# Kernel tuning notes

Measured on AMD Instinct MI355X. Metric: run time of the kernel, lower is better.

Reference implementation:

```python
import jax, jax.numpy as jnp
import numpy as np

B, L, D, H = 8, 1024, 1024, 16
DPH = D // H  # 64


def setup_inputs() -> dict:
    key = jax.random.key(0)
    ks = jax.random.split(key, 12)
    s = 1.0 / np.sqrt(D)
    return {
        "key": jax.random.normal(ks[0], (B, L, D), jnp.float32),
        "value": jax.random.normal(ks[1], (B, L, D), jnp.float32),
        "query": jax.random.normal(ks[2], (B, L, D), jnp.float32),
        "attn_mask": jax.random.randint(ks[3], (B, L, L), 0, 2) > 0,
        "Wq": jax.random.normal(ks[4], (D, D), jnp.float32) * s,
        "bq": jnp.zeros((D,), jnp.float32),
        "Wk": jax.random.normal(ks[5], (D, D), jnp.float32) * s,
        "bk": jnp.zeros((D,), jnp.float32),
        "Wv": jax.random.normal(ks[6], (D, D), jnp.float32) * s,
        "bv": jnp.zeros((D,), jnp.float32),
        "Wo": jax.random.normal(ks[7], (D, D), jnp.float32) * s,
        "bo": jnp.zeros((D,), jnp.float32),
        "gamma": jnp.ones((D,), jnp.float32),
        "beta": jnp.zeros((D,), jnp.float32),
    }


def _layer_norm(x, gamma, beta, eps=1e-5):
    mu = jnp.mean(x, axis=-1, keepdims=True)
    var = jnp.var(x, axis=-1, keepdims=True)
    return (x - mu) * jax.lax.rsqrt(var + eps) * gamma + beta


def reference(key, value, query, attn_mask, Wq, bq, Wk, bk, Wv, bv, Wo, bo, gamma, beta):
    residual = query
    k = key @ Wk + bk      # [B, L, D]
    v = value @ Wv + bv
    q = query @ Wq + bq
    # faithful to torch: raw row-major view into [B*H, L, dph] (NOT standard head transpose)
    k = k.reshape(B * H, -1, DPH)
    v = v.reshape(B * H, -1, DPH)
    q = q.reshape(B * H, -1, DPH)
    # faithful to torch repeat: tile whole batch H times along dim 0
    mask = jnp.tile(attn_mask, (H, 1, 1))  # [B*H, L, L]
    scale = DPH ** (-0.5)
    scores = jnp.einsum('bqd,bkd->bqk', q, k) * scale
    scores = jnp.where(mask, jnp.float32(-1e9), scores)
    attention = jax.nn.softmax(scores, axis=2)
    context = jnp.einsum('bqk,bkd->bqd', attention, v)  # [B*H, L, dph]
    context = context.reshape(B, -1, D)
    output = context @ Wo + bo
    output = _layer_norm(residual + output, gamma, beta)
    return (output, attention)
```

## Files before the change

### kernel.cpp

```cpp
#include <hip/hip_runtime.h>

typedef __attribute__((ext_vector_type(8))) short short8;
typedef __attribute__((ext_vector_type(4))) float f32x4;

#define AS1C(p) ((const __attribute__((address_space(1))) void*)(p))
#define AS3(p)  ((__attribute__((address_space(3))) void*)(p))

__device__ __forceinline__ unsigned short f2bf(float f) {
  unsigned int u = __float_as_uint(f);
  return (unsigned short)((u + 0x7fffu + ((u >> 16) & 1u)) >> 16);
}

__device__ __forceinline__ void gload16(const void* g, void* l) {
  __builtin_amdgcn_global_load_lds(AS1C(g), AS3(l), 16, 0, 0);
}

#define EXP_C 0.18033688011112042f

__global__ __launch_bounds__(256) void conv_bf16(const float* __restrict__ in,
                                                 unsigned short* __restrict__ out, int n4) {
  int i = blockIdx.x * 256 + threadIdx.x;
  if (i >= n4) return;
  float4 v = ((const float4*)in)[i];
  ushort4 o;
  o.x = f2bf(v.x); o.y = f2bf(v.y); o.z = f2bf(v.z); o.w = f2bf(v.w);
  ((ushort4*)out)[i] = o;
}

__global__ __launch_bounds__(256) void pack_mask_kernel(const int* __restrict__ m,
                                                        unsigned int* __restrict__ bits) {
  int i = blockIdx.x * 256 + threadIdx.x;
  unsigned long long b = __ballot(m[i] != 0);
  if ((threadIdx.x & 63) == 0) {
    bits[(i >> 5)]     = (unsigned int)b;
    bits[(i >> 5) + 1] = (unsigned int)(b >> 32);
  }
}

__global__ __launch_bounds__(256) void transpose_w(const float* __restrict__ W0,
                                                   const float* __restrict__ W1,
                                                   const float* __restrict__ W2,
                                                   const float* __restrict__ W3,
                                                   unsigned short* __restrict__ WtBase) {
  __shared__ float t[32][33];
  const float* W = (blockIdx.z == 0) ? W0 : (blockIdx.z == 1) ? W1 : (blockIdx.z == 2) ? W2 : W3;
  unsigned short* Wt = WtBase + (size_t)blockIdx.z * 1024 * 1024;
  int bx = blockIdx.x * 32, by = blockIdx.y * 32;
  int tx = threadIdx.x & 31, ty = threadIdx.x >> 5;
#pragma unroll
  for (int i = 0; i < 4; ++i) {
    int r = ty + i * 8;
    t[r][tx] = W[(size_t)(by + r) * 1024 + bx + tx];
  }
  __syncthreads();
#pragma unroll
  for (int i = 0; i < 4; ++i) {
    int r = ty + i * 8;
    Wt[(size_t)(bx + r) * 1024 + by + tx] = f2bf(t[tx][r]);
  }
}

__global__ __launch_bounds__(256) void transpose_v(const unsigned short* __restrict__ v,
                                                   unsigned short* __restrict__ vt) {
  __shared__ unsigned short t[32][33];
  int b = blockIdx.z;
  int bx = blockIdx.x * 32;
  int by = blockIdx.y * 32;
  int tx = threadIdx.x & 31, ty = threadIdx.x >> 5;
#pragma unroll
  for (int i = 0; i < 4; ++i) {
    int r = ty + i * 8;
    t[r][tx] = v[(size_t)b * 65536 + (size_t)(by + r) * 64 + bx + tx];
  }
  __syncthreads();
#pragma unroll
  for (int i = 0; i < 4; ++i) {
    int r = ty + i * 8;
    vt[(size_t)b * 65536 + (size_t)(bx + r) * 1024 + by + tx] = t[tx][r];
  }
}

template <int MODE>
__global__ __launch_bounds__(256) void gemm_bf16_kernel(
    const unsigned short* __restrict__ A, const unsigned short* __restrict__ Bt,
    const float* __restrict__ bias, const float* __restrict__ res,
    unsigned short* __restrict__ Cb, float* __restrict__ Cf) {
  const int K = 1024, N = 1024;
  __shared__ unsigned short lA[128 * 32];
  __shared__ unsigned short lB[128 * 32];
  const int tid = threadIdx.x;
  const int wave = tid >> 6, lane = tid & 63;
  const int row_l = lane & 15, kg = lane >> 4;
  const int wg = blockIdx.y * 8 + blockIdx.x;
  const int idx = (wg & 7) * 64 + (wg >> 3);
  const int m0 = (idx >> 3) * 128, n0 = (idx & 7) * 128;
  const int wm = (wave >> 1) * 64, wn = (wave & 1) * 64;
  f32x4 acc[4][4] = {};

  for (int k0 = 0; k0 < K; k0 += 32) {
    __syncthreads();
#pragma unroll
    for (int it = 0; it < 2; ++it) {
      int c = wave * 64 + it * 256 + lane;
      int r = c >> 2, ch = c & 3;
      int sch = ch ^ (r & 3);
      gload16(A + (size_t)(m0 + r) * K + k0 + sch * 8, lA + (wave * 64 + it * 256) * 8);
      gload16(Bt + (size_t)(n0 + r) * K + k0 + sch * 8, lB + (wave * 64 + it * 256) * 8);
    }
    __syncthreads();
    short8 af[4], bfr[4];
#pragma unroll
    for (int t = 0; t < 4; ++t) {
      int ra = wm + t * 16 + row_l;
      af[t] = *(const short8*)(lA + ra * 32 + ((kg ^ (ra & 3)) << 3));
      int rb = wn + t * 16 + row_l;
      bfr[t] = *(const short8*)(lB + rb * 32 + ((kg ^ (rb & 3)) << 3));
    }
    __builtin_amdgcn_s_setprio(1);
#pragma unroll
    for (int mt = 0; mt < 4; ++mt)
#pragma unroll
      for (int nt = 0; nt < 4; ++nt)
        acc[mt][nt] = __builtin_amdgcn_mfma_f32_16x16x32_bf16(af[mt], bfr[nt], acc[mt][nt], 0, 0, 0);
    __builtin_amdgcn_s_setprio(0);
  }
#pragma unroll
  for (int mt = 0; mt < 4; ++mt)
#pragma unroll
    for (int nt = 0; nt < 4; ++nt)
#pragma unroll
      for (int r = 0; r < 4; ++r) {
        int grow = m0 + wm + mt * 16 + kg * 4 + r;
        int gcol = n0 + wn + nt * 16 + row_l;
        float v = acc[mt][nt][r] + bias[gcol];
        if (MODE == 0) {
          Cb[(size_t)grow * N + gcol] = f2bf(v);
        } else {
          v += res[(size_t)grow * N + gcol];
          Cf[(size_t)grow * N + gcol] = v;
        }
      }
}

__global__ __launch_bounds__(256) void attn_kernel(
    const unsigned short* __restrict__ Q,
    const unsigned short* __restrict__ Km,
    const unsigned short* __restrict__ Vt,
    const unsigned int* __restrict__ mbits,
    float* __restrict__ attn,
    unsigned short* __restrict__ ctx) {
  __shared__ unsigned short lQ[64 * 64];
  __shared__ unsigned short lK[64 * 64];
  __shared__ unsigned short lV[64 * 64];
  __shared__ unsigned short lP[64 * 64];
  const int tid = threadIdx.x, wave = tid >> 6, lane = tid & 63;
  const int row_l = lane & 15, kg = lane >> 4;
  const int wg = blockIdx.y * 16 + blockIdx.x;
  const int idx = (wg & 7) * 256 + (wg >> 3);
  const int batch = idx >> 4, qt = idx & 15;
  const int q0 = qt * 64;
  const unsigned short* Qb = Q + (size_t)batch * 65536;
  const unsigned short* Kb = Km + (size_t)batch * 65536;
  const unsigned short* Vb = Vt + (size_t)batch * 65536;
  const unsigned int* mrow = mbits + (size_t)(batch & 7) * 32768;
  float* attb = attn + (size_t)batch * 1048576;

#pragma unroll
  for (int it = 0; it < 2; ++it) {
    int c = wave * 64 + it * 256 + lane;
    int r = c >> 3, ch = c & 7;
    int sch = ch ^ (r & 7);
    gload16(Qb + (size_t)(q0 + r) * 64 + sch * 8, lQ + (wave * 64 + it * 256) * 8);
  }
  __syncthreads();
  short8 qf[2];
  {
    int rq = wave * 16 + row_l;
#pragma unroll
    for (int kk = 0; kk < 2; ++kk)
      qf[kk] = *(const short8*)(lQ + rq * 64 + (((kk * 4 + kg) ^ (rq & 7)) << 3));
  }

  float l_part[4] = {0.f, 0.f, 0.f, 0.f};
  const int qrow_base = q0 + wave * 16 + kg * 4;

  for (int kt = 0; kt < 16; ++kt) {
    __syncthreads();
#pragma unroll
    for (int it = 0; it < 2; ++it) {
      int c = wave * 64 + it * 256 + lane;
      int r = c >> 3, ch = c & 7;
      int sch = ch ^ (r & 7);
      gload16(Kb + (size_t)(kt * 64 + r) * 64 + sch * 8, lK + (wave * 64 + it * 256) * 8);
    }
    __syncthreads();
    f32x4 s[4];
    __builtin_amdgcn_s_setprio(1);
#pragma unroll
    for (int cf = 0; cf < 4; ++cf) {
      int rk = cf * 16 + row_l;
      f32x4 a = {0.f, 0.f, 0.f, 0.f};
#pragma unroll
      for (int kk = 0; kk < 2; ++kk) {
        short8 kf = *(const short8*)(lK + rk * 64 + (((kk * 4 + kg) ^ (rk & 7)) << 3));
        a = __builtin_amdgcn_mfma_f32_16x16x32_bf16(qf[kk], kf, a, 0, 0, 0);
      }
      s[cf] = a;
    }
    __builtin_amdgcn_s_setprio(0);
#pragma unroll
    for (int r = 0; r < 4; ++r) {
      unsigned int w0 = mrow[(qrow_base + r) * 32 + kt * 2];
      unsigned int w1 = mrow[(qrow_base + r) * 32 + kt * 2 + 1];
#pragma unroll
      for (int cf = 0; cf < 4; ++cf) {
        int kl = cf * 16 + row_l;
        unsigned int w = (kl & 32) ? w1 : w0;
        int bit = (w >> (kl & 31)) & 1;
        float e = __builtin_exp2f(s[cf][r] * EXP_C);
        l_part[r] += bit ? 0.f : e;
      }
    }
  }
  float il[4];
#pragma unroll
  for (int r = 0; r < 4; ++r) {
    float se = l_part[r];
#pragma unroll
    for (int sh = 1; sh < 16; sh <<= 1) se += __shfl_xor(se, sh);
    il[r] = 1.f / se;
  }

  f32x4 cacc[4] = {};

  for (int kt = 0; kt < 16; ++kt) {
    __syncthreads();
#pragma unroll
    for (int it = 0; it < 2; ++it) {
      int c = wave * 64 + it * 256 + lane;
      int r = c >> 3, ch = c & 7;
      int sch = ch ^ (r & 7);
      gload16(Kb + (size_t)(kt * 64 + r) * 64 + sch * 8, lK + (wave * 64 + it * 256) * 8);
      gload16(Vb + (size_t)r * 1024 + kt * 64 + sch * 8, lV + (wave * 64 + it * 256) * 8);
    }
    __syncthreads();
    f32x4 s[4];
    __builtin_amdgcn_s_setprio(1);
#pragma unroll
    for (int cf = 0; cf < 4; ++cf) {
      int rk = cf * 16 + row_l;
      f32x4 a = {0.f, 0.f, 0.f, 0.f};
#pragma unroll
      for (int kk = 0; kk < 2; ++kk) {
        short8 kf = *(const short8*)(lK + rk * 64 + (((kk * 4 + kg) ^ (rk & 7)) << 3));
        a = __builtin_amdgcn_mfma_f32_16x16x32_bf16(qf[kk], kf, a, 0, 0, 0);
      }
      s[cf] = a;
    }
    __builtin_amdgcn_s_setprio(0);
#pragma unroll
    for (int r = 0; r < 4; ++r) {
      unsigned int w0 = mrow[(qrow_base + r) * 32 + kt * 2];
      unsigned int w1 = mrow[(qrow_base + r) * 32 + kt * 2 + 1];
      float* arow = attb + (size_t)(qrow_base + r) * 1024 + kt * 64;
      int prow = wave * 16 + kg * 4 + r;
#pragma unroll
      for (int cf = 0; cf < 4; ++cf) {
        int kl = cf * 16 + row_l;
        unsigned int w = (kl & 32) ? w1 : w0;
        int bit = (w >> (kl & 31)) & 1;
        float e = __builtin_exp2f(s[cf][r] * EXP_C) * il[r];
        float p = bit ? 0.f : e;
        __builtin_nontemporal_store(p, arow + kl);
        int pch = (kl >> 3) ^ (prow & 7);
        lP[prow * 64 + pch * 8 + (kl & 7)] = f2bf(p);
      }
    }
    __syncthreads();
    __builtin_amdgcn_s_setprio(1);
#pragma unroll
    for (int kk = 0; kk < 2; ++kk) {
      int rp = wave * 16 + row_l;
      short8 pa = *(const short8*)(lP + rp * 64 + (((kk * 4 + kg) ^ (rp & 7)) << 3));
#pragma unroll
      for (int df = 0; df < 4; ++df) {
        int rv = df * 16 + row_l;
        short8 vb = *(const short8*)(lV + rv * 64 + (((kk * 4 + kg) ^ (rv & 7)) << 3));
        cacc[df] = __builtin_amdgcn_mfma_f32_16x16x32_bf16(pa, vb, cacc[df], 0, 0, 0);
      }
    }
    __builtin_amdgcn_s_setprio(0);
  }
#pragma unroll
  for (int df = 0; df < 4; ++df)
#pragma unroll
    for (int r = 0; r < 4; ++r) {
      int grow = q0 + wave * 16 + kg * 4 + r;
      int gcol = df * 16 + row_l;
      ctx[(size_t)batch * 65536 + (size_t)grow * 64 + gcol] = f2bf(cacc[df][r]);
    }
}

__global__ __launch_bounds__(256) void layernorm_kernel(float* __restrict__ io,
                                                        const float* __restrict__ gamma,
                                                        const float* __restrict__ beta) {
  int wave = threadIdx.x >> 6, lane = threadIdx.x & 63;
  size_t row = (size_t)blockIdx.x * 4 + wave;
  float* p = io + row * 1024;
  float4 v[4];
  float s = 0.f, ss = 0.f;
#pragma unroll
  for (int i = 0; i < 4; ++i) {
    v[i] = ((const float4*)p)[lane + i * 64];
    s += v[i].x + v[i].y + v[i].z + v[i].w;
    ss += v[i].x * v[i].x + v[i].y * v[i].y + v[i].z * v[i].z + v[i].w * v[i].w;
  }
#pragma unroll
  for (int m = 1; m < 64; m <<= 1) { s += __shfl_xor(s, m); ss += __shfl_xor(ss, m); }
  float mu = s * (1.f / 1024.f);
  float var = ss * (1.f / 1024.f) - mu * mu;
  float rinv = rsqrtf(var + 1e-5f);
#pragma unroll
  for (int i = 0; i < 4; ++i) {
    int idx = lane + i * 64;
    float4 g = ((const float4*)gamma)[idx];
    float4 b = ((const float4*)beta)[idx];
    float4 o;
    o.x = (v[i].x - mu) * rinv * g.x + b.x;
    o.y = (v[i].y - mu) * rinv * g.y + b.y;
    o.z = (v[i].z - mu) * rinv * g.z + b.z;
    o.w = (v[i].w - mu) * rinv * g.w + b.w;
    ((float4*)p)[idx] = o;
  }
}

extern "C" void kernel_launch(void* const* d_in, const int* in_sizes, int n_in,
                              void* d_out, int out_size, void* d_ws, size_t ws_size,
                              hipStream_t stream) {
  const float* key   = (const float*)d_in[0];
  const float* value = (const float*)d_in[1];
  const float* query = (const float*)d_in[2];
  const int* amask   = (const int*)d_in[3];
  const float* Wq = (const float*)d_in[4];
  const float* bq = (const float*)d_in[5];
  const float* Wk = (const float*)d_in[6];
  const float* bk = (const float*)d_in[7];
  const float* Wv = (const float*)d_in[8];
  const float* bv = (const float*)d_in[9];
  const float* Wo = (const float*)d_in[10];
  const float* bo = (const float*)d_in[11];
  const float* gamma = (const float*)d_in[12];
  const float* beta  = (const float*)d_in[13];

  char* ws = (char*)d_ws;
  const size_t MB = 1024 * 1024;
  unsigned short* B0 = (unsigned short*)(ws + 0);
  unsigned short* B1 = (unsigned short*)(ws + 16 * MB);
  unsigned short* B2 = (unsigned short*)(ws + 32 * MB);
  unsigned short* B3 = (unsigned short*)(ws + 48 * MB);
  unsigned short* Wts = (unsigned short*)(ws + 64 * MB);
  unsigned int* mbits = (unsigned int*)(ws + 72 * MB);
  unsigned short* Wqt = Wts;
  unsigned short* Wkt = Wts + 1 * MB;
  unsigned short* Wvt = Wts + 2 * MB;
  unsigned short* Wot = Wts + 3 * MB;

  float* out_f = (float*)d_out;
  float* attn_f = (float*)d_out + (size_t)8388608;

  const int n4 = 8388608 / 4;
  dim3 gemm_grid(8, 64);

  transpose_w<<<dim3(32, 32, 4), 256, 0, stream>>>(Wq, Wk, Wv, Wo, Wts);
  pack_mask_kernel<<<32768, 256, 0, stream>>>(amask, mbits);

  conv_bf16<<<8192, 256, 0, stream>>>(query, B0, n4);
  gemm_bf16_kernel<0><<<gemm_grid, 256, 0, stream>>>(B0, Wqt, bq, nullptr, B1, nullptr);
  conv_bf16<<<8192, 256, 0, stream>>>(key, B0, n4);
  gemm_bf16_kernel<0><<<gemm_grid, 256, 0, stream>>>(B0, Wkt, bk, nullptr, B2, nullptr);
  conv_bf16<<<8192, 256, 0, stream>>>(value, B0, n4);
  gemm_bf16_kernel<0><<<gemm_grid, 256, 0, stream>>>(B0, Wvt, bv, nullptr, B3, nullptr);
  transpose_v<<<dim3(2, 32, 128), 256, 0, stream>>>(B3, B0);

  attn_kernel<<<dim3(16, 128), 256, 0, stream>>>(B1, B2, B0, mbits, attn_f, B3);

  gemm_bf16_kernel<1><<<gemm_grid, 256, 0, stream>>>(B3, Wot, bo, query, nullptr, out_f);
  layernorm_kernel<<<2048, 256, 0, stream>>>(out_f, gamma, beta);
}
```

Measured before the change: 360.7 us.

## Double-buffer attention K/V tiles, transpose mask bits, batch QKV GEMMs

Several changes are bundled. The attention kernel double-buffers K and V tiles in LDS so the next tile's loads overlap compute, and it replaces the paired __syncthreads with a vmcnt wait plus barrier. The packed mask is stored transposed so each thread fetches its four rows' words with one vector load. Attention probability writes are staged through LDS as bf16 and written as 16-byte nontemporal stores, which rounds the fp32 attention output to bf16 precision. When the workspace is large enough, the three input conversions and QKV GEMMs are merged into single launches over a z dimension.

Result: slower. 732.3 us (+103.0%).

```diff
diff --git a/kernel.cpp b/kernel.cpp
--- a/kernel.cpp
+++ b/kernel.cpp
@@ -10,6 +10,9 @@
   unsigned int u = __float_as_uint(f);
   return (unsigned short)((u + 0x7fffu + ((u >> 16) & 1u)) >> 16);
 }
+__device__ __forceinline__ float bf2f(short s) {
+  return __uint_as_float(((unsigned int)(unsigned short)s) << 16);
+}
 
 __device__ __forceinline__ void gload16(const void* g, void* l) {
   __builtin_amdgcn_global_load_lds(AS1C(g), AS3(l), 16, 0, 0);
@@ -17,8 +20,14 @@
 
 #define EXP_C 0.18033688011112042f
 
-__global__ __launch_bounds__(256) void conv_bf16(const float* __restrict__ in,
-                                                 unsigned short* __restrict__ out, int n4) {
+__global__ __launch_bounds__(256) void conv3_bf16(const float* __restrict__ s0,
+                                                  const float* __restrict__ s1,
+                                                  const float* __restrict__ s2,
+                                                  unsigned short* __restrict__ d0,
+                                                  unsigned short* __restrict__ d1,
+                                                  unsigned short* __restrict__ d2, int n4) {
+  const float* in = (blockIdx.z == 0) ? s0 : (blockIdx.z == 1) ? s1 : s2;
+  unsigned short* out = (blockIdx.z == 0) ? d0 : (blockIdx.z == 1) ? d1 : d2;
   int i = blockIdx.x * 256 + threadIdx.x;
   if (i >= n4) return;
   float4 v = ((const float4*)in)[i];
@@ -28,12 +37,14 @@
 }
 
 __global__ __launch_bounds__(256) void pack_mask_kernel(const int* __restrict__ m,
-                                                        unsigned int* __restrict__ bits) {
+                                                        unsigned int* __restrict__ bitsT) {
   int i = blockIdx.x * 256 + threadIdx.x;
-  unsigned long long b = __ballot(m[i] != 0);
+  unsigned long long bl = __ballot(m[i] != 0);
   if ((threadIdx.x & 63) == 0) {
-    bits[(i >> 5)]     = (unsigned int)b;
-    bits[(i >> 5) + 1] = (unsigned int)(b >> 32);
+    int b_ = i >> 20, q = (i >> 10) & 1023, k = i & 1023;
+    int w = k >> 5;
+    bitsT[b_ * 32768 + w * 1024 + q]       = (unsigned int)bl;
+    bitsT[b_ * 32768 + (w + 1) * 1024 + q] = (unsigned int)(bl >> 32);
   }
 }
 
@@ -81,13 +92,12 @@
 }
 
 template <int MODE>
-__global__ __launch_bounds__(256) void gemm_bf16_kernel(
+__device__ __forceinline__ void gemm_body(
     const unsigned short* __restrict__ A, const unsigned short* __restrict__ Bt,
     const float* __restrict__ bias, const float* __restrict__ res,
-    unsigned short* __restrict__ Cb, float* __restrict__ Cf) {
+    unsigned short* __restrict__ Cb, float* __restrict__ Cf,
+    unsigned short* lA, unsigned short* lB) {
   const int K = 1024, N = 1024;
-  __shared__ unsigned short lA[128 * 32];
-  __shared__ unsigned short lB[128 * 32];
   const int tid = threadIdx.x;
   const int wave = tid >> 6, lane = tid & 63;
   const int row_l = lane & 15, kg = lane >> 4;
@@ -142,17 +152,39 @@
       }
 }
 
+__global__ __launch_bounds__(256) void gemm_qkv_kernel(
+    const unsigned short* __restrict__ A0, const unsigned short* __restrict__ A1,
+    const unsigned short* __restrict__ A2, const unsigned short* __restrict__ WtBase,
+    const float* __restrict__ b0, const float* __restrict__ b1, const float* __restrict__ b2,
+    unsigned short* __restrict__ C0, unsigned short* __restrict__ C1,
+    unsigned short* __restrict__ C2) {
+  __shared__ unsigned short lA[128 * 32];
+  __shared__ unsigned short lB[128 * 32];
+  int z = blockIdx.z;
+  const unsigned short* A = (z == 0) ? A0 : (z == 1) ? A1 : A2;
+  const float* bias = (z == 0) ? b0 : (z == 1) ? b1 : b2;
+  unsigned short* C = (z == 0) ? C0 : (z == 1) ? C1 : C2;
+  gemm_body<0>(A, WtBase + (size_t)z * 1024 * 1024, bias, nullptr, C, nullptr, lA, lB);
+}
+
+__global__ __launch_bounds__(256) void gemm_out_kernel(
+    const unsigned short* __restrict__ A, const unsigned short* __restrict__ Bt,
+    const float* __restrict__ bias, const float* __restrict__ res, float* __restrict__ Cf) {
+  __shared__ unsigned short lA[128 * 32];
+  __shared__ unsigned short lB[128 * 32];
+  gemm_body<1>(A, Bt, bias, res, nullptr, Cf, lA, lB);
+}
+
 __global__ __launch_bounds__(256) void attn_kernel(
     const unsigned short* __restrict__ Q,
     const unsigned short* __restrict__ Km,
     const unsigned short* __restrict__ Vt,
-    const unsigned int* __restrict__ mbits,
+    const unsigned int* __restrict__ mbitsT,
     float* __restrict__ attn,
     unsigned short* __restrict__ ctx) {
-  __shared__ unsigned short lQ[64 * 64];
-  __shared__ unsigned short lK[64 * 64];
-  __shared__ unsigned short lV[64 * 64];
-  __shared__ unsigned short lP[64 * 64];
+  __shared__ unsigned short lQP[64 * 64];
+  __shared__ unsigned short lK[2][64 * 64];
+  __shared__ unsigned short lV[2][64 * 64];
   const int tid = threadIdx.x, wave = tid >> 6, lane = tid & 63;
   const int row_l = lane & 15, kg = lane >> 4;
   const int wg = blockIdx.y * 16 + blockIdx.x;
@@ -162,38 +194,57 @@
   const unsigned short* Qb = Q + (size_t)batch * 65536;
   const unsigned short* Kb = Km + (size_t)batch * 65536;
   const unsigned short* Vb = Vt + (size_t)batch * 65536;
-  const unsigned int* mrow = mbits + (size_t)(batch & 7) * 32768;
+  const unsigned int* mT = mbitsT + (size_t)(batch & 7) * 32768;
   float* attb = attn + (size_t)batch * 1048576;
+  const int qrow_base = q0 + wave * 16 + kg * 4;
+
+#define STAGE_K(kt, buf)                                                              \
+  {                                                                                   \
+    _Pragma("unroll") for (int it = 0; it < 2; ++it) {                                \
+      int c = wave * 64 + it * 256 + lane;                                            \
+      int r_ = c >> 3, ch_ = c & 7, sch_ = ch_ ^ (r_ & 7);                            \
+      gload16(Kb + (size_t)((kt) * 64 + r_) * 64 + sch_ * 8,                          \
+              lK[buf] + (wave * 64 + it * 256) * 8);                                  \
+    }                                                                                 \
+  }
+#define STAGE_V(kt, buf)                                                              \
+  {                                                                                   \
+    _Pragma("unroll") for (int it = 0; it < 2; ++it) {                                \
+      int c = wave * 64 + it * 256 + lane;                                            \
+      int r_ = c >> 3, ch_ = c & 7, sch_ = ch_ ^ (r_ & 7);                            \
+      gload16(Vb + (size_t)r_ * 1024 + (kt) * 64 + sch_ * 8,                          \
+              lV[buf] + (wave * 64 + it * 256) * 8);                                  \
+    }                                                                                 \
+  }
+#define WAIT_BAR                                              \
+  asm volatile("s_waitcnt vmcnt(0)" ::: "memory");            \
+  __builtin_amdgcn_s_barrier();
 
 #pragma unroll
   for (int it = 0; it < 2; ++it) {
     int c = wave * 64 + it * 256 + lane;
     int r = c >> 3, ch = c & 7;
     int sch = ch ^ (r & 7);
-    gload16(Qb + (size_t)(q0 + r) * 64 + sch * 8, lQ + (wave * 64 + it * 256) * 8);
-  }
-  __syncthreads();
+    gload16(Qb + (size_t)(q0 + r) * 64 + sch * 8, lQP + (wave * 64 + it * 256) * 8);
+  }
+  STAGE_K(0, 0)
+  WAIT_BAR
   short8 qf[2];
   {
     int rq = wave * 16 + row_l;
 #pragma unroll
     for (int kk = 0; kk < 2; ++kk)
-      qf[kk] = *(const short8*)(lQ + rq * 64 + (((kk * 4 + kg) ^ (rq & 7)) << 3));
+      qf[kk] = *(const short8*)(lQP + rq * 64 + (((kk * 4 + kg) ^ (rq & 7)) << 3));
   }
 
   float l_part[4] = {0.f, 0.f, 0.f, 0.f};
-  const int qrow_base = q0 + wave * 16 + kg * 4;
 
   for (int kt = 0; kt < 16; ++kt) {
-    __syncthreads();
-#pragma unroll
-    for (int it = 0; it < 2; ++it) {
-      int c = wave * 64 + it * 256 + lane;
-      int r = c >> 3, ch = c & 7;
-      int sch = ch ^ (r & 7);
-      gload16(Kb + (size_t)(kt * 64 + r) * 64 + sch * 8, lK + (wave * 64 + it * 256) * 8);
-    }
-    __syncthreads();
+    int cur = kt & 1;
+    if (kt < 15) STAGE_K(kt + 1, cur ^ 1)
+    uint4 mw0 = *(const uint4*)(mT + (kt * 2 + 0) * 1024 + qrow_base);
+    uint4 mw1 = *(const uint4*)(mT + (kt * 2 + 1) * 1024 + qrow_base);
+    unsigned int wv[2][4] = {{mw0.x, mw0.y, mw0.z, mw0.w}, {mw1.x, mw1.y, mw1.z, mw1.w}};
     f32x4 s[4];
     __builtin_amdgcn_s_setprio(1);
 #pragma unroll
@@ -202,25 +253,21 @@
       f32x4 a = {0.f, 0.f, 0.f, 0.f};
 #pragma unroll
       for (int kk = 0; kk < 2; ++kk) {
-        short8 kf = *(const short8*)(lK + rk * 64 + (((kk * 4 + kg) ^ (rk & 7)) << 3));
+        short8 kf = *(const short8*)(lK[cur] + rk * 64 + (((kk * 4 + kg) ^ (rk & 7)) << 3));
         a = __builtin_amdgcn_mfma_f32_16x16x32_bf16(qf[kk], kf, a, 0, 0, 0);
       }
       s[cf] = a;
     }
     __builtin_amdgcn_s_setprio(0);
 #pragma unroll
-    for (int r = 0; r < 4; ++r) {
-      unsigned int w0 = mrow[(qrow_base + r) * 32 + kt * 2];
-      unsigned int w1 = mrow[(qrow_base + r) * 32 + kt * 2 + 1];
+    for (int r = 0; r < 4; ++r)
 #pragma unroll
       for (int cf = 0; cf < 4; ++cf) {
-        int kl = cf * 16 + row_l;
-        unsigned int w = (kl & 32) ? w1 : w0;
-        int bit = (w >> (kl & 31)) & 1;
+        int bit = (wv[cf >> 1][r] >> ((cf & 1) * 16 + row_l)) & 1;
         float e = __builtin_exp2f(s[cf][r] * EXP_C);
         l_part[r] += bit ? 0.f : e;
       }
-    }
+    WAIT_BAR
   }
   float il[4];
 #pragma unroll
@@ -232,18 +279,20 @@
   }
 
   f32x4 cacc[4] = {};
-
+  unsigned short* lP = lQP;
+
+  STAGE_K(0, 0)
+  STAGE_V(0, 0)
+  WAIT_BAR
   for (int kt = 0; kt < 16; ++kt) {
-    __syncthreads();
-#pragma unroll
-    for (int it = 0; it < 2; ++it) {
-      int c = wave * 64 + it * 256 + lane;
-      int r = c >> 3, ch = c & 7;
-      int sch = ch ^ (r & 7);
-      gload16(Kb + (size_t)(kt * 64 + r) * 64 + sch * 8, lK + (wave * 64 + it * 256) * 8);
-      gload16(Vb + (size_t)r * 1024 + kt * 64 + sch * 8, lV + (wave * 64 + it * 256) * 8);
-    }
-    __syncthreads();
+    int cur = kt & 1;
+    if (kt < 15) {
+      STAGE_K(kt + 1, cur ^ 1)
+      STAGE_V(kt + 1, cur ^ 1)
+    }
+    uint4 mw0 = *(const uint4*)(mT + (kt * 2 + 0) * 1024 + qrow_base);
+    uint4 mw1 = *(const uint4*)(mT + (kt * 2 + 1) * 1024 + qrow_base);
+    unsigned int wv[2][4] = {{mw0.x, mw0.y, mw0.z, mw0.w}, {mw1.x, mw1.y, mw1.z, mw1.w}};
     f32x4 s[4];
     __builtin_amdgcn_s_setprio(1);
 #pragma unroll
@@ -252,7 +301,7 @@
       f32x4 a = {0.f, 0.f, 0.f, 0.f};
 #pragma unroll
       for (int kk = 0; kk < 2; ++kk) {
-        short8 kf = *(const short8*)(lK + rk * 64 + (((kk * 4 + kg) ^ (rk & 7)) << 3));
+        short8 kf = *(const short8*)(lK[cur] + rk * 64 + (((kk * 4 + kg) ^ (rk & 7)) << 3));
         a = __builtin_amdgcn_mfma_f32_16x16x32_bf16(qf[kk], kf, a, 0, 0, 0);
       }
       s[cf] = a;
@@ -260,23 +309,33 @@
     __builtin_amdgcn_s_setprio(0);
 #pragma unroll
     for (int r = 0; r < 4; ++r) {
-      unsigned int w0 = mrow[(qrow_base + r) * 32 + kt * 2];
-      unsigned int w1 = mrow[(qrow_base + r) * 32 + kt * 2 + 1];
-      float* arow = attb + (size_t)(qrow_base + r) * 1024 + kt * 64;
       int prow = wave * 16 + kg * 4 + r;
 #pragma unroll
       for (int cf = 0; cf < 4; ++cf) {
         int kl = cf * 16 + row_l;
-        unsigned int w = (kl & 32) ? w1 : w0;
-        int bit = (w >> (kl & 31)) & 1;
+        int bit = (wv[cf >> 1][r] >> ((cf & 1) * 16 + row_l)) & 1;
         float e = __builtin_exp2f(s[cf][r] * EXP_C) * il[r];
         float p = bit ? 0.f : e;
-        __builtin_nontemporal_store(p, arow + kl);
         int pch = (kl >> 3) ^ (prow & 7);
         lP[prow * 64 + pch * 8 + (kl & 7)] = f2bf(p);
       }
     }
-    __syncthreads();
+    {
+      int pr = wave * 16 + kg * 4 + (row_l & 3);
+      int cb = row_l >> 2;
+      float* arow = attb + (size_t)(q0 + pr) * 1024 + kt * 64 + cb * 16;
+      int ch0 = (cb * 2) ^ (pr & 7), ch1 = (cb * 2 + 1) ^ (pr & 7);
+      short8 a0 = *(const short8*)(lP + pr * 64 + ch0 * 8);
+      short8 a1 = *(const short8*)(lP + pr * 64 + ch1 * 8);
+      f32x4 o0 = {bf2f(a0[0]), bf2f(a0[1]), bf2f(a0[2]), bf2f(a0[3])};
+      f32x4 o1 = {bf2f(a0[4]), bf2f(a0[5]), bf2f(a0[6]), bf2f(a0[7])};
+      f32x4 o2 = {bf2f(a1[0]), bf2f(a1[1]), bf2f(a1[2]), bf2f(a1[3])};
+      f32x4 o3 = {bf2f(a1[4]), bf2f(a1[5]), bf2f(a1[6]), bf2f(a1[7])};
+      __builtin_nontemporal_store(o0, (f32x4*)arow + 0);
+      __builtin_nontemporal_store(o1, (f32x4*)arow + 1);
+      __builtin_nontemporal_store(o2, (f32x4*)arow + 2);
+      __builtin_nontemporal_store(o3, (f32x4*)arow + 3);
+    }
     __builtin_amdgcn_s_setprio(1);
 #pragma unroll
     for (int kk = 0; kk < 2; ++kk) {
@@ -285,11 +344,12 @@
 #pragma unroll
       for (int df = 0; df < 4; ++df) {
         int rv = df * 16 + row_l;
-        short8 vb = *(const short8*)(lV + rv * 64 + (((kk * 4 + kg) ^ (rv & 7)) << 3));
+        short8 vb = *(const short8*)(lV[cur] + rv * 64 + (((kk * 4 + kg) ^ (rv & 7)) << 3));
         cacc[df] = __builtin_amdgcn_mfma_f32_16x16x32_bf16(pa, vb, cacc[df], 0, 0, 0);
       }
     }
     __builtin_amdgcn_s_setprio(0);
+    WAIT_BAR
   }
 #pragma unroll
   for (int df = 0; df < 4; ++df)
@@ -299,6 +359,9 @@
       int gcol = df * 16 + row_l;
       ctx[(size_t)batch * 65536 + (size_t)grow * 64 + gcol] = f2bf(cacc[df][r]);
     }
+#undef STAGE_K
+#undef STAGE_V
+#undef WAIT_BAR
 }
 
 __global__ __launch_bounds__(256) void layernorm_kernel(float* __restrict__ io,
@@ -354,36 +417,50 @@
 
   char* ws = (char*)d_ws;
   const size_t MB = 1024 * 1024;
-  unsigned short* B0 = (unsigned short*)(ws + 0);
-  unsigned short* B1 = (unsigned short*)(ws + 16 * MB);
-  unsigned short* B2 = (unsigned short*)(ws + 32 * MB);
-  unsigned short* B3 = (unsigned short*)(ws + 48 * MB);
-  unsigned short* Wts = (unsigned short*)(ws + 64 * MB);
-  unsigned int* mbits = (unsigned int*)(ws + 72 * MB);
-  unsigned short* Wqt = Wts;
-  unsigned short* Wkt = Wts + 1 * MB;
-  unsigned short* Wvt = Wts + 2 * MB;
-  unsigned short* Wot = Wts + 3 * MB;
-
   float* out_f = (float*)d_out;
   float* attn_f = (float*)d_out + (size_t)8388608;
-
   const int n4 = 8388608 / 4;
   dim3 gemm_grid(8, 64);
-
-  transpose_w<<<dim3(32, 32, 4), 256, 0, stream>>>(Wq, Wk, Wv, Wo, Wts);
-  pack_mask_kernel<<<32768, 256, 0, stream>>>(amask, mbits);
-
-  conv_bf16<<<8192, 256, 0, stream>>>(query, B0, n4);
-  gemm_bf16_kernel<0><<<gemm_grid, 256, 0, stream>>>(B0, Wqt, bq, nullptr, B1, nullptr);
-  conv_bf16<<<8192, 256, 0, stream>>>(key, B0, n4);
-  gemm_bf16_kernel<0><<<gemm_grid, 256, 0, stream>>>(B0, Wkt, bk, nullptr, B2, nullptr);
-  conv_bf16<<<8192, 256, 0, stream>>>(value, B0, n4);
-  gemm_bf16_kernel<0><<<gemm_grid, 256, 0, stream>>>(B0, Wvt, bv, nullptr, B3, nullptr);
-  transpose_v<<<dim3(2, 32, 128), 256, 0, stream>>>(B3, B0);
-
-  attn_kernel<<<dim3(16, 128), 256, 0, stream>>>(B1, B2, B0, mbits, attn_f, B3);
-
-  gemm_bf16_kernel<1><<<gemm_grid, 256, 0, stream>>>(B3, Wot, bo, query, nullptr, out_f);
-  layernorm_kernel<<<2048, 256, 0, stream>>>(out_f, gamma, beta);
-}
+  dim3 gemm_grid3(8, 64, 3);
+
+  const bool fused = ws_size >= 106 * MB;
+  if (fused) {
+    unsigned short* A0 = (unsigned short*)(ws + 0);
+    unsigned short* A1 = (unsigned short*)(ws + 16 * MB);
+    unsigned short* A2 = (unsigned short*)(ws + 32 * MB);
+    unsigned short* B1 = (unsigned short*)(ws + 48 * MB);
+    unsigned short* B2 = (unsigned short*)(ws + 64 * MB);
+    unsigned short* B3 = (unsigned short*)(ws + 80 * MB);
+    unsigned short* Wts = (unsigned short*)(ws + 96 * MB);
+    unsigned int* mbitsT = (unsigned int*)(ws + 104 * MB);
+
+    transpose_w<<<dim3(32, 32, 4), 256, 0, stream>>>(Wq, Wk, Wv, Wo, Wts);
+    pack_mask_kernel<<<32768, 256, 0, stream>>>(amask, mbitsT);
+    conv3_bf16<<<dim3(8192, 1, 3), 256, 0, stream>>>(query, key, value, A0, A1, A2, n4);
+    gemm_qkv_kernel<<<gemm_grid3, 256, 0, stream>>>(A0, A1, A2, Wts, bq, bk, bv, B1, B2, B3);
+    transpose_v<<<dim3(2, 32, 128), 256, 0, stream>>>(B3, A0);
+    attn_kernel<<<dim3(16, 128), 256, 0, stream>>>(B1, B2, A0, mbitsT, attn_f, B3);
+    gemm_out_kernel<<<gemm_grid, 256, 0, stream>>>(B3, Wts + 3 * MB, bo, query, out_f);
+    layernorm_kernel<<<2048, 256, 0, stream>>>(out_f, gamma, beta);
+  } else {
+    unsigned short* B0 = (unsigned short*)(ws + 0);
+    unsigned short* B1 = (unsigned short*)(ws + 16 * MB);
+    unsigned short* B2 = (unsigned short*)(ws + 32 * MB);
+    unsigned short* B3 = (unsigned short*)(ws + 48 * MB);
+    unsigned short* Wts = (unsigned short*)(ws + 64 * MB);
+    unsigned int* mbitsT = (unsigned int*)(ws + 72 * MB);
+
+    transpose_w<<<dim3(32, 32, 4), 256, 0, stream>>>(Wq, Wk, Wv, Wo, Wts);
+    pack_mask_kernel<<<32768, 256, 0, stream>>>(amask, mbitsT);
+    conv3_bf16<<<dim3(8192, 1, 1), 256, 0, stream>>>(query, query, query, B0, B0, B0, n4);
+    gemm_qkv_kernel<<<gemm_grid, 256, 0, stream>>>(B0, B0, B0, Wts, bq, bq, bq, B1, B1, B1);
+    conv3_bf16<<<dim3(8192, 1, 1), 256, 0, stream>>>(key, key, key, B0, B0, B0, n4);
+    gemm_qkv_kernel<<<gemm_grid, 256, 0, stream>>>(B0, B0, B0, Wts + 1 * MB, bk, bk, bk, B2, B2, B2);
+    conv3_bf16<<<dim3(8192, 1, 1), 256, 0, stream>>>(value, value, value, B0, B0, B0, n4);
+    gemm_qkv_kernel<<<gemm_grid, 256, 0, stream>>>(B0, B0, B0, Wts + 2 * MB, bv, bv, bv, B3, B3, B3);
+    transpose_v<<<dim3(2, 32, 128), 256, 0, stream>>>(B3, B0);
+    attn_kernel<<<dim3(16, 128), 256, 0, stream>>>(B1, B2, B0, mbitsT, attn_f, B3);
+    gemm_out_kernel<<<gemm_grid, 256, 0, stream>>>(B3, Wts + 3 * MB, bo, query, out_f);
+    layernorm_kernel<<<2048, 256, 0, stream>>>(out_f, gamma, beta);
+  }
+}
```
